# Performance work log

Measured on AMD Instinct MI355X. Metric: run time of the kernel, lower is better.

The kernel has to match this reference:

```python
import jax, jax.numpy as jnp
import numpy as np

N = 50000          # num nodes
EDG = 1600000      # num edges
DIM = 128          # in_dim == out_dim (dim_h)
H = 8              # num_heads
HD = DIM // H      # head dim = 16
BN_EPS = 1e-5


def _batchnorm(x, gamma, beta):
    # training-mode BatchNorm1d: biased batch stats over node axis
    mean = x.mean(axis=0)
    var = x.var(axis=0)
    return (x - mean) * jax.lax.rsqrt(var + BN_EPS) * gamma + beta


def setup_inputs() -> dict:
    key = jax.random.key(0)
    ks = jax.random.split(key, 12)
    lin = lambda k, o, i: jax.random.normal(k, (o, i), jnp.float32) * (1.0 / np.sqrt(i))
    return {
        "h": jax.random.normal(ks[0], (N, DIM), jnp.float32),
        "edge_index": jax.random.randint(ks[1], (2, EDG), 0, N, jnp.int32),
        "edge_attr": jax.random.normal(ks[2], (EDG, DIM), jnp.float32),
        "Wq": lin(ks[3], DIM, DIM),
        "Wk": lin(ks[4], DIM, DIM),
        "Wv": lin(ks[5], DIM, DIM),
        "We": lin(ks[6], DIM, DIM),
        "Wb": lin(ks[7], H, DIM),
        "bb": jnp.zeros((H,), jnp.float32),
        "gamma1": jnp.ones((DIM,), jnp.float32),
        "beta1": jnp.zeros((DIM,), jnp.float32),
        "W1": lin(ks[8], 2 * DIM, DIM),
        "b1": jnp.zeros((2 * DIM,), jnp.float32),
        "W2": lin(ks[9], DIM, 2 * DIM),
        "b2": jnp.zeros((DIM,), jnp.float32),
        "gamma2": jnp.ones((DIM,), jnp.float32),
        "beta2": jnp.zeros((DIM,), jnp.float32),
    }


def reference(h, edge_index, edge_attr, Wq, Wk, Wv, We, Wb, bb,
              gamma1, beta1, W1, b1, W2, b2, gamma2, beta2):
    n = h.shape[0]
    src, dst = edge_index[0], edge_index[1]

    Qh = (h @ Wq.T).reshape(n, H, HD)
    Kh = (h @ Wk.T).reshape(n, H, HD)
    Vh = (h @ Wv.T).reshape(n, H, HD)
    E = (edge_attr @ We.T).reshape(-1, H, HD)          # (EDG, H, HD)
    E_bias = edge_attr @ Wb.T + bb                      # (EDG, H)

    # per-edge attention score: sum over head dim of Kh[src]*Qh[dst]*E
    score = (Kh[src] * Qh[dst] * E).sum(-1) / np.sqrt(HD) + E_bias
    score = jnp.exp(jnp.clip(score, -5.0, 5.0))         # (EDG, H)

    msg = Vh[src] * score[..., None]                    # (EDG, H, HD)
    wV = jax.ops.segment_sum(msg, dst, num_segments=n)  # (N, H, HD)
    Z = jax.ops.segment_sum(score, dst, num_segments=n) # (N, H)

    h_attn = (wV / (Z[..., None] + 1e-6)).reshape(n, DIM)
    x = h + h_attn                                      # residual
    x = _batchnorm(x, gamma1, beta1)

    ff = jax.nn.relu(x @ W1.T + b1) @ W2.T + b2
    out = _batchnorm(x + ff, gamma2, beta2)
    return out
```

## Files before the change

### kernel.cpp

```cpp
#include <hip/hip_runtime.h>
#include <math.h>

typedef __attribute__((ext_vector_type(8))) short bf16x8;
typedef __attribute__((ext_vector_type(4))) short bf16x4;
typedef __attribute__((ext_vector_type(4))) float f32x4;

static __device__ __forceinline__ unsigned short f2bf(float x){
    union{float f; unsigned u;} v; v.f = x;
    unsigned r = v.u + 0x7fffu + ((v.u >> 16) & 1u);
    return (unsigned short)(r >> 16);
}
static __device__ __forceinline__ unsigned cvtpk(float lo, float hi){
    unsigned r;
    asm("v_cvt_pk_bf16_f32 %0, %1, %2" : "=v"(r) : "v"(lo), "v"(hi));
    return r;
}
static __device__ __forceinline__ float bflo(unsigned u){
    union{unsigned x; float f;} v; v.x = u << 16; return v.f;
}
static __device__ __forceinline__ float bfhi(unsigned u){
    union{unsigned x; float f;} v; v.x = u & 0xffff0000u; return v.f;
}

__global__ __launch_bounds__(128)
void qkv_kernel(const float* __restrict__ h,
                const float* __restrict__ Wq, const float* __restrict__ Wk,
                const float* __restrict__ Wv,
                float* __restrict__ Qb, unsigned short* __restrict__ Kb16,
                unsigned short* __restrict__ Vb16)
{
    __shared__ float hl[16 * 128];
    const int t  = threadIdx.x;
    const int n0 = blockIdx.x * 16;

    const float4* hg4 = (const float4*)(h + (size_t)n0 * 128);
    float4* hl4 = (float4*)hl;
    #pragma unroll
    for (int i = 0; i < 4; ++i) hl4[i * 128 + t] = hg4[i * 128 + t];
    __syncthreads();

    #pragma unroll
    for (int m = 0; m < 3; ++m) {
        const float* W = (m == 0 ? Wq : (m == 1 ? Wk : Wv)) + t * 128;
        float acc[16];
        #pragma unroll
        for (int n = 0; n < 16; ++n) acc[n] = 0.f;
        for (int kc = 0; kc < 32; ++kc) {
            const float4 w = *(const float4*)(W + kc * 4);
            #pragma unroll
            for (int n = 0; n < 16; ++n) {
                const float4 x = *(const float4*)&hl[n * 128 + kc * 4];
                acc[n] += w.x * x.x + w.y * x.y + w.z * x.z + w.w * x.w;
            }
        }
        if (m == 0) {
            float* o = Qb + (size_t)n0 * 128 + t;
            #pragma unroll
            for (int n = 0; n < 16; ++n) o[(size_t)n * 128] = acc[n];
        } else {
            unsigned short* o = (m == 1 ? Kb16 : Vb16) + (size_t)n0 * 128 + t;
            #pragma unroll
            for (int n = 0; n < 16; ++n) o[(size_t)n * 128] = f2bf(acc[n]);
        }
    }
}

__global__ void hist_kernel(const int* __restrict__ ei, int* __restrict__ cnt, int EDG)
{
    const int stride = gridDim.x * blockDim.x;
    for (int e = blockIdx.x * blockDim.x + threadIdx.x; e < EDG; e += stride)
        atomicAdd(&cnt[ei[EDG + e]], 1);
}

__global__ __launch_bounds__(1024)
void scan_a(const int* __restrict__ cnt, int* __restrict__ bsum, int n)
{
    __shared__ int tmp[1024];
    const int t = threadIdx.x;
    const int i = blockIdx.x * 1024 + t;
    tmp[t] = (i < n) ? cnt[i] : 0;
    __syncthreads();
    for (int d = 512; d > 0; d >>= 1) {
        if (t < d) tmp[t] += tmp[t + d];
        __syncthreads();
    }
    if (t == 0) bsum[blockIdx.x] = tmp[0];
}

__global__ void scan_b(const int* __restrict__ bsum, int* __restrict__ bbase,
                       int* __restrict__ offs, int nb, int n)
{
    if (threadIdx.x == 0) {
        int run = 0;
        for (int b = 0; b < nb; ++b) { bbase[b] = run; run += bsum[b]; }
        offs[n] = run;
    }
}

__global__ __launch_bounds__(1024)
void scan_c(const int* __restrict__ cnt, const int* __restrict__ bbase,
            int* __restrict__ offs, int n)
{
    __shared__ int tmp[1024];
    const int t = threadIdx.x;
    const int i = blockIdx.x * 1024 + t;
    const int v = (i < n) ? cnt[i] : 0;
    tmp[t] = v;
    __syncthreads();
    for (int d = 1; d < 1024; d <<= 1) {
        const int a = (t >= d) ? tmp[t - d] : 0;
        __syncthreads();
        tmp[t] += a;
        __syncthreads();
    }
    if (i < n) offs[i] = bbase[blockIdx.x] + tmp[t] - v;
}

__global__ void scatter_kernel(const int* __restrict__ ei, const int* __restrict__ offs,
                               int* __restrict__ cnt, int2* __restrict__ elist, int EDG)
{
    const int stride = gridDim.x * blockDim.x;
    for (int e = blockIdx.x * blockDim.x + threadIdx.x; e < EDG; e += stride) {
        const int d = ei[EDG + e];
        const int p = atomicSub(&cnt[d], 1) - 1;
        int2 v; v.x = ei[e]; v.y = e;
        elist[offs[d] + p] = v;
    }
}

__global__ __launch_bounds__(256, 3)
void fused_attn(const float* __restrict__ eattr, const int2* __restrict__ elist,
                const int* __restrict__ offs,
                const float* __restrict__ We, const float* __restrict__ Wb,
                const float* __restrict__ bbv,
                const float* __restrict__ Qb, const unsigned short* __restrict__ Kb16,
                const unsigned short* __restrict__ Vb16, const float* __restrict__ h,
                float* __restrict__ x, float* __restrict__ stat, int N, int EDG)
{
    __shared__ unsigned short WeB[128 * 128];
    __shared__ unsigned short WbB[16 * 128];
    __shared__ float scw[4][16][8];
    __shared__ int   srw[4][16];

    const int t = threadIdx.x;
    #pragma unroll
    for (int i = 0; i < 16; ++i) {
        const int idx4 = i * 256 + t;
        const int d = idx4 >> 5, k0 = (idx4 & 31) * 4;
        const float4 wv = *(const float4*)&We[d * 128 + k0];
        bf16x4 p;
        p[0] = (short)f2bf(wv.x); p[1] = (short)f2bf(wv.y);
        p[2] = (short)f2bf(wv.z); p[3] = (short)f2bf(wv.w);
        *(bf16x4*)((char*)WeB + d * 256 + ((2 * k0) ^ ((d & 7) << 4))) = p;
    }
    #pragma unroll
    for (int i = 0; i < 8; ++i) {
        const int idx = i * 256 + t;
        const int r = idx >> 7, k = idx & 127;
        const unsigned short v = (r < 8) ? f2bf(Wb[r * 128 + k]) : (unsigned short)0;
        *(unsigned short*)((char*)WbB + r * 256 + ((2 * k) ^ ((r & 7) << 4))) = v;
    }
    __syncthreads();

    const int l = t & 63, w = t >> 6;
    const int eloc = l & 15, g4 = l >> 4;
    const int half = l >> 5, q = l & 31;
    const int hq = q >> 2;
    const int kb_l = g4 * 16;
    float bb[8];
    #pragma unroll
    for (int hh = 0; hh < 8; ++hh) bb[hh] = bbv[hh];

    float4 sA = {0.f, 0.f, 0.f, 0.f}, sQ2 = {0.f, 0.f, 0.f, 0.f};
    const int GW = gridDim.x * 4;
    for (int node = blockIdx.x * 4 + w; node < N; node += GW) {
        const int beg = offs[node], end = offs[node + 1];

        const float* qrow = Qb + (size_t)node * 128 + g4 * 4;
        float4 qv[8];
        #pragma unroll
        for (int hh = 0; hh < 8; ++hh) qv[hh] = *(const float4*)(qrow + hh * 16);

        int2 se;
        float4 ea0[4], ea1[4];
        {
            const int ii = min(beg + eloc, EDG - 1);
            se = elist[ii];
            const float* ep = eattr + (size_t)se.y * 128 + g4 * 8;
            #pragma unroll
            for (int ks = 0; ks < 4; ++ks) {
                ea0[ks] = *(const float4*)(ep + ks * 32);
                ea1[ks] = *(const float4*)(ep + ks * 32 + 4);
            }
        }

        float4 pv = {0.f, 0.f, 0.f, 0.f};
        float zz = 0.f;

        for (int base = beg; base < end; base += 16) {
            const int cnt = min(16, end - base);
            const unsigned short* kr16 = Kb16 + (size_t)se.x * 128 + g4 * 4;
            const bool havenext = (base + 16 < end);

            int2 se2 = se;
            if (havenext) se2 = elist[min(base + 16 + eloc, EDG - 1)];

            f32x4 acc[8], accb;
            #pragma unroll
            for (int hh = 0; hh < 8; ++hh) acc[hh] = (f32x4){0.f, 0.f, 0.f, 0.f};
            accb = (f32x4){0.f, 0.f, 0.f, 0.f};
            #pragma unroll
            for (int ks = 0; ks < 4; ++ks) {
                union { unsigned u[4]; bf16x8 v; } fr;
                fr.u[0] = cvtpk(ea0[ks].x, ea0[ks].y);
                fr.u[1] = cvtpk(ea0[ks].z, ea0[ks].w);
                fr.u[2] = cvtpk(ea1[ks].x, ea1[ks].y);
                fr.u[3] = cvtpk(ea1[ks].z, ea1[ks].w);
                const int kb = ks * 64 + kb_l;
                const bf16x8 abf = *(const bf16x8*)((char*)WbB + eloc * 256 + (kb ^ ((eloc & 7) << 4)));
                accb = __builtin_amdgcn_mfma_f32_16x16x32_bf16(abf, fr.v, accb, 0, 0, 0);
                #pragma unroll
                for (int hh = 0; hh < 8; ++hh) {
                    const int ar = hh * 16 + eloc;
                    const bf16x8 af = *(const bf16x8*)((char*)WeB + ar * 256 + (kb ^ ((ar & 7) << 4)));
                    acc[hh] = __builtin_amdgcn_mfma_f32_16x16x32_bf16(af, fr.v, acc[hh], 0, 0, 0);
                }
            }

            if (havenext) {
                const float* ep2 = eattr + (size_t)se2.y * 128 + g4 * 8;
                #pragma unroll
                for (int ks = 0; ks < 4; ++ks) {
                    ea0[ks] = *(const float4*)(ep2 + ks * 32);
                    ea1[ks] = *(const float4*)(ep2 + ks * 32 + 4);
                }
            }

            float scv[8];
            #pragma unroll
            for (int hh = 0; hh < 8; ++hh) {
                const uint2 k2 = *(const uint2*)(kr16 + hh * 16);
                const float4 qq = qv[hh];
                float m = acc[hh][0] * (bflo(k2.x) * qq.x)
                        + acc[hh][1] * (bfhi(k2.x) * qq.y)
                        + acc[hh][2] * (bflo(k2.y) * qq.z)
                        + acc[hh][3] * (bfhi(k2.y) * qq.w);
                m += __shfl_xor(m, 16);
                m += __shfl_xor(m, 32);
                const float eb = __shfl(accb[hh & 3], ((hh >> 2) << 4) | eloc);
                float sc = m * 0.25f + eb + bb[hh];
                sc = expf(fminf(fmaxf(sc, -5.f), 5.f));
                scv[hh] = (eloc < cnt) ? sc : 0.f;
            }
            if (l < 16) {
                float4 s0 = {scv[0], scv[1], scv[2], scv[3]};
                float4 s1 = {scv[4], scv[5], scv[6], scv[7]};
                *(float4*)&scw[w][l][0] = s0;
                *(float4*)&scw[w][l][4] = s1;
                srw[w][l] = se.x;
            }
            asm volatile("s_waitcnt lgkmcnt(0)" ::: "memory");
            __builtin_amdgcn_sched_barrier(0);

            int e = half;
            for (; e + 2 < cnt; e += 4) {
                const int   s0 = srw[w][e],     s1 = srw[w][e + 2];
                const float c0 = scw[w][e][hq], c1 = scw[w][e + 2][hq];
                const uint2 u0 = *(const uint2*)(Vb16 + (size_t)s0 * 128 + 4 * q);
                const uint2 u1 = *(const uint2*)(Vb16 + (size_t)s1 * 128 + 4 * q);
                pv.x += bflo(u0.x) * c0 + bflo(u1.x) * c1;
                pv.y += bfhi(u0.x) * c0 + bfhi(u1.x) * c1;
                pv.z += bflo(u0.y) * c0 + bflo(u1.y) * c1;
                pv.w += bfhi(u0.y) * c0 + bfhi(u1.y) * c1;
                zz += c0 + c1;
            }
            for (; e < cnt; e += 2) {
                const int   s0 = srw[w][e];
                const float c0 = scw[w][e][hq];
                const uint2 u0 = *(const uint2*)(Vb16 + (size_t)s0 * 128 + 4 * q);
                pv.x += bflo(u0.x) * c0; pv.y += bfhi(u0.x) * c0;
                pv.z += bflo(u0.y) * c0; pv.w += bfhi(u0.y) * c0;
                zz += c0;
            }
            se = se2;
        }

        pv.x += __shfl_xor(pv.x, 32); pv.y += __shfl_xor(pv.y, 32);
        pv.z += __shfl_xor(pv.z, 32); pv.w += __shfl_xor(pv.w, 32);
        zz   += __shfl_xor(zz, 32);
        if (half == 0) {
            const float inv = 1.f / (zz + 1e-6f);
            const float4 hv = *(const float4*)&h[(size_t)node * 128 + 4 * q];
            float4 xv;
            xv.x = hv.x + pv.x * inv; xv.y = hv.y + pv.y * inv;
            xv.z = hv.z + pv.z * inv; xv.w = hv.w + pv.w * inv;
            *(float4*)&x[(size_t)node * 128 + 4 * q] = xv;
            sA.x += xv.x; sA.y += xv.y; sA.z += xv.z; sA.w += xv.w;
            sQ2.x += xv.x * xv.x; sQ2.y += xv.y * xv.y;
            sQ2.z += xv.z * xv.z; sQ2.w += xv.w * xv.w;
        }
    }

    __syncthreads();
    float* wbF = (float*)WbB;
    if (half == 0) {
        *(float4*)&wbF[w * 256 + 4 * q]       = sA;
        *(float4*)&wbF[w * 256 + 128 + 4 * q] = sQ2;
    }
    __syncthreads();
    if (t < 128) {
        float s = 0.f, sq2 = 0.f;
        #pragma unroll
        for (int wi = 0; wi < 4; ++wi) {
            s   += wbF[wi * 256 + t];
            sq2 += wbF[wi * 256 + 128 + t];
        }
        atomicAdd(&stat[t], s);
        atomicAdd(&stat[128 + t], sq2);
    }
}

__global__ void bn_params(const float* __restrict__ sum, const float* __restrict__ sumsq,
                          const float* __restrict__ gamma, const float* __restrict__ beta,
                          float* __restrict__ a, float* __restrict__ b, float invn)
{
    const int c = threadIdx.x;
    const float mean = sum[c] * invn;
    const float var  = sumsq[c] * invn - mean * mean;
    const float sc   = gamma[c] * rsqrtf(var + 1e-5f);
    a[c] = sc;
    b[c] = beta[c] - mean * sc;
}

__global__ __launch_bounds__(128)
void ffn_kernel(const float* __restrict__ x, const float* __restrict__ W1,
                const float* __restrict__ b1, const float* __restrict__ W2,
                const float* __restrict__ b2, const float* __restrict__ par,
                float* __restrict__ zb, float* __restrict__ stat2)
{
    __shared__ float xnl[16 * 128];
    __shared__ float hidl[16 * 256];
    const int t  = threadIdx.x;
    const int n0 = blockIdx.x * 16;

    const float4* xg4 = (const float4*)(x + (size_t)n0 * 128);
    const float4* a4  = (const float4*)par;
    const float4* bv4 = (const float4*)(par + 128);
    float4* xnl4 = (float4*)xnl;
    #pragma unroll
    for (int i = 0; i < 4; ++i) {
        const int idx = i * 128 + t;
        const float4 xv = xg4[idx];
        const float4 av = a4[idx & 31], bv = bv4[idx & 31];
        float4 r;
        r.x = xv.x * av.x + bv.x; r.y = xv.y * av.y + bv.y;
        r.z = xv.z * av.z + bv.z; r.w = xv.w * av.w + bv.w;
        xnl4[idx] = r;
    }
    __syncthreads();

    float acc0[16], acc1[16];
    #pragma unroll
    for (int n = 0; n < 16; ++n) { acc0[n] = 0.f; acc1[n] = 0.f; }
    const float* w0p = W1 + (size_t)t * 128;
    const float* w1p = W1 + (size_t)(t + 128) * 128;
    for (int kc = 0; kc < 32; ++kc) {
        const float4 w0 = *(const float4*)(w0p + kc * 4);
        const float4 w1 = *(const float4*)(w1p + kc * 4);
        #pragma unroll
        for (int n = 0; n < 16; ++n) {
            const float4 xv = *(const float4*)&xnl[n * 128 + kc * 4];
            acc0[n] += w0.x * xv.x + w0.y * xv.y + w0.z * xv.z + w0.w * xv.w;
            acc1[n] += w1.x * xv.x + w1.y * xv.y + w1.z * xv.z + w1.w * xv.w;
        }
    }
    const float bi0 = b1[t], bi1 = b1[t + 128];
    #pragma unroll
    for (int n = 0; n < 16; ++n) {
        hidl[n * 256 + t]       = fmaxf(acc0[n] + bi0, 0.f);
        hidl[n * 256 + 128 + t] = fmaxf(acc1[n] + bi1, 0.f);
    }
    __syncthreads();

    float acc2[16];
    #pragma unroll
    for (int n = 0; n < 16; ++n) acc2[n] = 0.f;
    const float* w2p = W2 + (size_t)t * 256;
    for (int kc = 0; kc < 64; ++kc) {
        const float4 w = *(const float4*)(w2p + kc * 4);
        #pragma unroll
        for (int n = 0; n < 16; ++n) {
            const float4 hv = *(const float4*)&hidl[n * 256 + kc * 4];
            acc2[n] += w.x * hv.x + w.y * hv.y + w.z * hv.z + w.w * hv.w;
        }
    }
    const float bi2 = b2[t];
    float s = 0.f, sq = 0.f;
    float* zo = zb + (size_t)n0 * 128 + t;
    #pragma unroll
    for (int n = 0; n < 16; ++n) {
        const float z = xnl[n * 128 + t] + acc2[n] + bi2;
        zo[(size_t)n * 128] = z;
        s += z; sq += z * z;
    }
    atomicAdd(&stat2[t], s);
    atomicAdd(&stat2[128 + t], sq);
}

__global__ void final_bn(const float4* __restrict__ zb, const float* __restrict__ pa,
                         const float* __restrict__ pb, float4* __restrict__ out, int total4)
{
    const float4* a4 = (const float4*)pa;
    const float4* b4 = (const float4*)pb;
    const int stride = gridDim.x * blockDim.x;
    for (int i = blockIdx.x * blockDim.x + threadIdx.x; i < total4; i += stride) {
        const float4 z = zb[i];
        const float4 a = a4[i & 31], b = b4[i & 31];
        float4 r;
        r.x = z.x * a.x + b.x; r.y = z.y * a.y + b.y;
        r.z = z.z * a.z + b.z; r.w = z.w * a.w + b.w;
        out[i] = r;
    }
}

extern "C" void kernel_launch(void* const* d_in, const int* in_sizes, int n_in,
                              void* d_out, int out_size, void* d_ws, size_t ws_size,
                              hipStream_t stream)
{
    const float* h   = (const float*)d_in[0];
    const int*   ei  = (const int*)  d_in[1];
    const float* ea  = (const float*)d_in[2];
    const float* Wq  = (const float*)d_in[3];
    const float* Wk  = (const float*)d_in[4];
    const float* Wv  = (const float*)d_in[5];
    const float* We  = (const float*)d_in[6];
    const float* Wb  = (const float*)d_in[7];
    const float* bbv = (const float*)d_in[8];
    const float* g1  = (const float*)d_in[9];
    const float* be1 = (const float*)d_in[10];
    const float* W1  = (const float*)d_in[11];
    const float* b1  = (const float*)d_in[12];
    const float* W2  = (const float*)d_in[13];
    const float* b2  = (const float*)d_in[14];
    const float* g2  = (const float*)d_in[15];
    const float* be2 = (const float*)d_in[16];
    float* out = (float*)d_out;

    const int N   = in_sizes[0] / 128;
    const int EDG = in_sizes[1] / 2;
    const int NB  = (N + 1023) / 1024;
    const size_t nd = (size_t)N * 128;
    auto al8 = [](size_t v){ return (v + 7) & ~(size_t)7; };

    float* ws = (float*)d_ws;
    const size_t Qo  = 0;
    const size_t K16 = nd;
    const size_t V16 = nd + nd / 2;
    const size_t Xo  = 2 * nd;
    const size_t ELo = 3 * nd;
    const size_t OFo = ELo + (size_t)EDG * 2;
    const size_t CUo = al8(OFo + (size_t)N + 8);
    const size_t BSo = al8(CUo + (size_t)N);
    const size_t BBo = al8(BSo + (size_t)NB);
    const size_t STo = al8(BBo + (size_t)NB);
    const size_t PAR = STo + 512;

    int*  cnt   = (int*)(ws + CUo);
    int*  offs  = (int*)(ws + OFo);
    int*  bsum  = (int*)(ws + BSo);
    int*  bbase = (int*)(ws + BBo);
    int2* elist = (int2*)(ws + ELo);
    unsigned short* kb16 = (unsigned short*)(ws + K16);
    unsigned short* vb16 = (unsigned short*)(ws + V16);

    hipMemsetAsync(cnt, 0, (size_t)N * sizeof(int), stream);
    hipMemsetAsync(ws + STo, 0, 512 * sizeof(float), stream);

    qkv_kernel<<<N / 16, 128, 0, stream>>>(h, Wq, Wk, Wv, ws + Qo, kb16, vb16);

    hist_kernel<<<1024, 256, 0, stream>>>(ei, cnt, EDG);
    scan_a<<<NB, 1024, 0, stream>>>(cnt, bsum, N);
    scan_b<<<1, 64, 0, stream>>>(bsum, bbase, offs, NB, N);
    scan_c<<<NB, 1024, 0, stream>>>(cnt, bbase, offs, N);
    scatter_kernel<<<1024, 256, 0, stream>>>(ei, offs, cnt, elist, EDG);

    fused_attn<<<1024, 256, 0, stream>>>(ea, elist, offs, We, Wb, bbv,
                                         ws + Qo, kb16, vb16, h,
                                         ws + Xo, ws + STo, N, EDG);

    bn_params<<<1, 128, 0, stream>>>(ws + STo, ws + STo + 128, g1, be1,
                                     ws + PAR, ws + PAR + 128, 1.0f / (float)N);
    ffn_kernel<<<N / 16, 128, 0, stream>>>(ws + Xo, W1, b1, W2, b2, ws + PAR,
                                           ws + Qo, ws + STo + 256);
    bn_params<<<1, 128, 0, stream>>>(ws + STo + 256, ws + STo + 384, g2, be2,
                                     ws + PAR + 256, ws + PAR + 384, 1.0f / (float)N);
    final_bn<<<1024, 256, 0, stream>>>((const float4*)(ws + Qo), ws + PAR + 256,
                                       ws + PAR + 384, (float4*)out, N * 32);
}
```

Before: 1.176 ms.

## Cut register pressure in fused attention by staging Q in LDS and splitting heads

Q rows now go through a small LDS buffer instead of 8 float4 registers. The edge-attr software prefetch of the next 16-edge chunk is dropped, so each chunk loads and converts its own edge attributes. The eight per-head MFMA accumulators are split into two passes of four. This lowers VGPR usage, presumably to support the 3-waves occupancy target, at the cost of exposing edge_attr load latency and adding LDS reads per head.

```diff
diff --git a/kernel.cpp b/kernel.cpp
--- a/kernel.cpp
+++ b/kernel.cpp
@@ -141,6 +141,7 @@
     __shared__ unsigned short WbB[16 * 128];
     __shared__ float scw[4][16][8];
     __shared__ int   srw[4][16];
+    __shared__ float qlds[4][128];
 
     const int t = threadIdx.x;
     #pragma unroll
@@ -167,98 +168,84 @@
     const int half = l >> 5, q = l & 31;
     const int hq = q >> 2;
     const int kb_l = g4 * 16;
-    float bb[8];
-    #pragma unroll
-    for (int hh = 0; hh < 8; ++hh) bb[hh] = bbv[hh];
 
     float4 sA = {0.f, 0.f, 0.f, 0.f}, sQ2 = {0.f, 0.f, 0.f, 0.f};
     const int GW = gridDim.x * 4;
     for (int node = blockIdx.x * 4 + w; node < N; node += GW) {
         const int beg = offs[node], end = offs[node + 1];
 
-        const float* qrow = Qb + (size_t)node * 128 + g4 * 4;
-        float4 qv[8];
-        #pragma unroll
-        for (int hh = 0; hh < 8; ++hh) qv[hh] = *(const float4*)(qrow + hh * 16);
-
-        int2 se;
-        float4 ea0[4], ea1[4];
-        {
-            const int ii = min(beg + eloc, EDG - 1);
-            se = elist[ii];
-            const float* ep = eattr + (size_t)se.y * 128 + g4 * 8;
-            #pragma unroll
-            for (int ks = 0; ks < 4; ++ks) {
-                ea0[ks] = *(const float4*)(ep + ks * 32);
-                ea1[ks] = *(const float4*)(ep + ks * 32 + 4);
-            }
-        }
+        *(float2*)&qlds[w][2 * l] = *(const float2*)&Qb[(size_t)node * 128 + 2 * l];
+        asm volatile("s_waitcnt lgkmcnt(0)" ::: "memory");
+        __builtin_amdgcn_sched_barrier(0);
 
         float4 pv = {0.f, 0.f, 0.f, 0.f};
         float zz = 0.f;
 
         for (int base = beg; base < end; base += 16) {
             const int cnt = min(16, end - base);
-            const unsigned short* kr16 = Kb16 + (size_t)se.x * 128 + g4 * 4;
-            const bool havenext = (base + 16 < end);
-
-            int2 se2 = se;
-            if (havenext) se2 = elist[min(base + 16 + eloc, EDG - 1)];
-
-            f32x4 acc[8], accb;
-            #pragma unroll
-            for (int hh = 0; hh < 8; ++hh) acc[hh] = (f32x4){0.f, 0.f, 0.f, 0.f};
-            accb = (f32x4){0.f, 0.f, 0.f, 0.f};
-            #pragma unroll
-            for (int ks = 0; ks < 4; ++ks) {
-                union { unsigned u[4]; bf16x8 v; } fr;
-                fr.u[0] = cvtpk(ea0[ks].x, ea0[ks].y);
-                fr.u[1] = cvtpk(ea0[ks].z, ea0[ks].w);
-                fr.u[2] = cvtpk(ea1[ks].x, ea1[ks].y);
-                fr.u[3] = cvtpk(ea1[ks].z, ea1[ks].w);
-                const int kb = ks * 64 + kb_l;
-                const bf16x8 abf = *(const bf16x8*)((char*)WbB + eloc * 256 + (kb ^ ((eloc & 7) << 4)));
-                accb = __builtin_amdgcn_mfma_f32_16x16x32_bf16(abf, fr.v, accb, 0, 0, 0);
+            const int ii = min(base + eloc, EDG - 1);
+            const int2 se = elist[ii];
+
+            bf16x8 frv[4];
+            {
+                const float* ep = eattr + (size_t)se.y * 128 + g4 * 8;
                 #pragma unroll
-                for (int hh = 0; hh < 8; ++hh) {
-                    const int ar = hh * 16 + eloc;
-                    const bf16x8 af = *(const bf16x8*)((char*)WeB + ar * 256 + (kb ^ ((ar & 7) << 4)));
-                    acc[hh] = __builtin_amdgcn_mfma_f32_16x16x32_bf16(af, fr.v, acc[hh], 0, 0, 0);
+                for (int ks = 0; ks < 4; ++ks) {
+                    const float4 a0 = *(const float4*)(ep + ks * 32);
+                    const float4 a1 = *(const float4*)(ep + ks * 32 + 4);
+                    union { unsigned u[4]; bf16x8 v; } fr;
+                    fr.u[0] = cvtpk(a0.x, a0.y);
+                    fr.u[1] = cvtpk(a0.z, a0.w);
+                    fr.u[2] = cvtpk(a1.x, a1.y);
+                    fr.u[3] = cvtpk(a1.z, a1.w);
+                    frv[ks] = fr.v;
                 }
             }
-
-            if (havenext) {
-                const float* ep2 = eattr + (size_t)se2.y * 128 + g4 * 8;
+            const unsigned short* kr16 = Kb16 + (size_t)se.x * 128 + g4 * 4;
+
+            f32x4 accb = (f32x4){0.f, 0.f, 0.f, 0.f};
+            #pragma unroll
+            for (int hp = 0; hp < 2; ++hp) {
+                f32x4 acc[4];
+                #pragma unroll
+                for (int h2 = 0; h2 < 4; ++h2) acc[h2] = (f32x4){0.f, 0.f, 0.f, 0.f};
                 #pragma unroll
                 for (int ks = 0; ks < 4; ++ks) {
-                    ea0[ks] = *(const float4*)(ep2 + ks * 32);
-                    ea1[ks] = *(const float4*)(ep2 + ks * 32 + 4);
+                    const int kb = ks * 64 + kb_l;
+                    if (hp == 0) {
+                        const bf16x8 abf = *(const bf16x8*)((char*)WbB + eloc * 256 + (kb ^ ((eloc & 7) << 4)));
+                        accb = __builtin_amdgcn_mfma_f32_16x16x32_bf16(abf, frv[ks], accb, 0, 0, 0);
+                    }
+                    #pragma unroll
+                    for (int h2 = 0; h2 < 4; ++h2) {
+                        const int ar = (hp * 4 + h2) * 16 + eloc;
+                        const bf16x8 af = *(const bf16x8*)((char*)WeB + ar * 256 + (kb ^ ((ar & 7) << 4)));
+                        acc[h2] = __builtin_amdgcn_mfma_f32_16x16x32_bf16(af, frv[ks], acc[h2], 0, 0, 0);
+                    }
+                }
+                float scv[4];
+                #pragma unroll
+                for (int h2 = 0; h2 < 4; ++h2) {
+                    const int hh = hp * 4 + h2;
+                    const uint2  k2 = *(const uint2*)(kr16 + hh * 16);
+                    const float4 q4 = *(const float4*)&qlds[w][hh * 16 + g4 * 4];
+                    float m = acc[h2][0] * (bflo(k2.x) * q4.x)
+                            + acc[h2][1] * (bfhi(k2.x) * q4.y)
+                            + acc[h2][2] * (bflo(k2.y) * q4.z)
+                            + acc[h2][3] * (bfhi(k2.y) * q4.w);
+                    m += __shfl_xor(m, 16);
+                    m += __shfl_xor(m, 32);
+                    const float eb = __shfl(accb[hh & 3], ((hh >> 2) << 4) | eloc);
+                    float sc = m * 0.25f + eb + bbv[hh];
+                    sc = expf(fminf(fmaxf(sc, -5.f), 5.f));
+                    scv[h2] = (eloc < cnt) ? sc : 0.f;
+                }
+                if (l < 16) {
+                    float4 s4 = {scv[0], scv[1], scv[2], scv[3]};
+                    *(float4*)&scw[w][l][hp * 4] = s4;
                 }
             }
-
-            float scv[8];
-            #pragma unroll
-            for (int hh = 0; hh < 8; ++hh) {
-                const uint2 k2 = *(const uint2*)(kr16 + hh * 16);
-                const float4 qq = qv[hh];
-                float m = acc[hh][0] * (bflo(k2.x) * qq.x)
-                        + acc[hh][1] * (bfhi(k2.x) * qq.y)
-                        + acc[hh][2] * (bflo(k2.y) * qq.z)
-                        + acc[hh][3] * (bfhi(k2.y) * qq.w);
-                m += __shfl_xor(m, 16);
-                m += __shfl_xor(m, 32);
-                const float eb = __shfl(accb[hh & 3], ((hh >> 2) << 4) | eloc);
-                float sc = m * 0.25f + eb + bb[hh];
-                sc = expf(fminf(fmaxf(sc, -5.f), 5.f));
-                scv[hh] = (eloc < cnt) ? sc : 0.f;
-            }
-            if (l < 16) {
-                float4 s0 = {scv[0], scv[1], scv[2], scv[3]};
-                float4 s1 = {scv[4], scv[5], scv[6], scv[7]};
-                *(float4*)&scw[w][l][0] = s0;
-                *(float4*)&scw[w][l][4] = s1;
-                srw[w][l] = se.x;
-            }
+            if (l < 16) srw[w][l] = se.x;
             asm volatile("s_waitcnt lgkmcnt(0)" ::: "memory");
             __builtin_amdgcn_sched_barrier(0);
 
@@ -282,7 +269,6 @@
                 pv.z += bflo(u0.y) * c0; pv.w += bfhi(u0.y) * c0;
                 zz += c0;
             }
-            se = se2;
         }
 
         pv.x += __shfl_xor(pv.x, 32); pv.y += __shfl_xor(pv.y, 32);
```

After: 1.196 ms. About the same (+1.7%).
